# Optimization experiments

Measured on AMD Instinct MI355X. Metric: run time of the kernel, lower is better.

Reference implementation:

```python
import jax, jax.numpy as jnp
import numpy as np

B, D, H, O = 4096, 1024, 8192, 1000

def _l2norm_rows(w):
    return w / jnp.maximum(jnp.linalg.norm(w, axis=1, keepdims=True), 1e-12)

def setup_inputs() -> dict:
    key = jax.random.key(0)
    k1, k2, k3 = jax.random.split(key, 3)
    x = jax.random.normal(k1, (B, D), dtype=jnp.float32)
    kohonen_weights = _l2norm_rows(jax.random.normal(k2, (H, D), dtype=jnp.float32))
    grossberg_weights = _l2norm_rows(jax.random.normal(k3, (O, H), dtype=jnp.float32))
    return {"x": x, "kohonen_weights": kohonen_weights, "grossberg_weights": grossberg_weights}

def reference(x, kohonen_weights, grossberg_weights):
    # x: [B, D] (already flat), kohonen_weights: [H, D], grossberg_weights: [O, H]
    x2 = jnp.sum(x * x, axis=1, keepdims=True)              # [B, 1]
    w2 = jnp.sum(kohonen_weights * kohonen_weights, axis=1)  # [H]
    # Euclidean cdist via the expanded quadratic form (same as torch.cdist p=2)
    sq = x2 + w2[None, :] - 2.0 * (x @ kohonen_weights.T)    # [B, H]
    distances = jnp.sqrt(jnp.maximum(sq, 0.0))
    winners = jnp.argmin(distances, axis=1)                  # [B] int
    # one_hot @ grossberg_weights.T is exactly a row gather of grossberg_weights.T
    output = jnp.take(grossberg_weights.T, winners, axis=0)  # [B, O]
    return (output, winners)
```

## Files before the change

kernel.cpp:

```cpp
#include <hip/hip_runtime.h>
#include <hip/hip_bf16.h>
#include <hip/hip_fp16.h>


#define BB 4096
#define DD 1024
#define HH 8192
#define OO 1000

#define BM 256
#define BN 128
#define BK 64
#define NTILES (HH / BN)

typedef _Float16 f16;
typedef float f32x4 __attribute__((ext_vector_type(4)));

typedef __attribute__((address_space(3))) uint32_t lds_u32_t;
typedef __attribute__((address_space(1))) uint32_t glb_u32_t;

__device__ __forceinline__ uint32_t packkey(float v, int col) {
  uint32_t u = __float_as_uint(v);
  uint32_t mask = (uint32_t)((int32_t)u >> 31) | 0x80000000u;
  u ^= mask;
  return (u & 0xFFFFFF80u) | (uint32_t)col;
}
__device__ __forceinline__ float unpackval(uint32_t k) {
  uint32_t u = k & 0xFFFFFF80u;
  uint32_t mask = (k & 0x80000000u) ? 0x80000000u : 0xFFFFFFFFu;
  return __uint_as_float(u ^ mask);
}
__device__ __forceinline__ void kmerge(uint32_t& k1, uint32_t& k2,
                                       uint32_t o1, uint32_t o2) {
  uint32_t mn = min(k1, o1);
  uint32_t alt = (k1 > o1) ? k2 : o2;
  k1 = max(k1, o1);
  k2 = max(mn, alt);
}

__global__ __launch_bounds__(256) void cvt_kernel(
    const float* __restrict__ x, const float* __restrict__ kw,
    uint8_t* __restrict__ xq, uint8_t* __restrict__ kq,
    const float* __restrict__ G, float* __restrict__ Gt) {
  const int tid = threadIdx.x;
  const int blk = blockIdx.x;
  __shared__ float tile[32][33];
  if (blk < (BB + HH) / 4) {
#pragma unroll
    for (int i = 0; i < 4; ++i) {
      int r = blk * 4 + i;
      const float* src = (r < BB) ? (x + (size_t)r * DD)
                                  : (kw + (size_t)(r - BB) * DD);
      uint8_t* dst = (r < BB) ? (xq + (size_t)r * DD)
                              : (kq + (size_t)(r - BB) * DD);
      float4 v = ((const float4*)src)[tid];
      int p = 0;
      p = __builtin_amdgcn_cvt_pk_fp8_f32(v.x, v.y, p, false);
      p = __builtin_amdgcn_cvt_pk_fp8_f32(v.z, v.w, p, true);
      ((int*)dst)[tid] = p;
    }
  } else {
    if (Gt == nullptr) return;
    const int tb = blk - (BB + HH) / 4;
    const int tx = tid & 31;
    const int ty = tid >> 5;
#pragma unroll 1
    for (int j4 = 0; j4 < 4; ++j4) {
      int tile_id = tb * 4 + j4;
      int h0 = (tile_id >> 5) * 32;
      int o0 = (tile_id & 31) * 32;
      __syncthreads();
#pragma unroll
      for (int j = 0; j < 4; ++j) {
        int o = o0 + ty + j * 8;
        if (o < OO) tile[ty + j * 8][tx] = G[(size_t)o * HH + h0 + tx];
      }
      __syncthreads();
#pragma unroll
      for (int j = 0; j < 4; ++j) {
        int o = o0 + tx;
        int h = h0 + ty + j * 8;
        if (o < OO) Gt[(size_t)h * OO + o] = tile[tx][ty + j * 8];
      }
    }
  }
}

__global__ __launch_bounds__(256, 2) void gemm_top2(
    const uint8_t* __restrict__ A, const uint8_t* __restrict__ Bt,
    uint4* __restrict__ pk) {
  __shared__ __align__(16) uint8_t sA[BM * BK];
  __shared__ __align__(16) uint8_t sB[BN * BK];
  __shared__ uint2 mk[BM][2];

  const int tid = threadIdx.x;
  const int w = tid >> 6;
  const int L = tid & 63;

  const int bid = blockIdx.y * gridDim.x + blockIdx.x;
  const int c8 = bid & 7;
  const int tt = bid >> 3;
  const int nx = c8 * 8 + (tt & 7);
  const int my = tt >> 3;
  const int m0 = my * BM;
  const int n0 = nx * BN;

  const int wr = w >> 1;
  const int wc = w & 1;

  f32x4 acc[8][4];
#pragma unroll
  for (int i = 0; i < 8; ++i)
#pragma unroll
    for (int j = 0; j < 4; ++j) {
      acc[i][j][0] = 0.f; acc[i][j][1] = 0.f; acc[i][j][2] = 0.f; acc[i][j][3] = 0.f;
    }

  const int lm = L & 15;
  const int lq = L >> 4;

  const uint8_t* pA[4]; int dA[4];
#pragma unroll
  for (int j = 0; j < 4; ++j) {
    int c = tid + 256 * j;
    int r = c >> 2;
    int so = ((c & 3) ^ ((r >> 1) & 3)) * 16;
    pA[j] = A + (size_t)(m0 + r) * DD + so;
    dA[j] = c * 16;
  }
  const uint8_t* pB[2]; int dB[2];
#pragma unroll
  for (int j = 0; j < 2; ++j) {
    int c = tid + 256 * j;
    int r = c >> 2;
    int so = ((c & 3) ^ ((r >> 1) & 3)) * 16;
    pB[j] = Bt + (size_t)(n0 + r) * DD + so;
    dB[j] = c * 16;
  }

  const int t2 = (lm >> 1) & 3;
  const int raBase = (wr * 128 + lm) * BK;
  const int rbBase = (wc * 64 + lm) * BK;
  const int off0 = (((lq >> 1)) ^ t2) * 16 + (lq & 1) * 8;
  const int off1 = ((2 + (lq >> 1)) ^ t2) * 16 + (lq & 1) * 8;

  for (int kt = 0; kt < DD / BK; ++kt) {
    __syncthreads();
#pragma unroll
    for (int j = 0; j < 4; ++j) {
      __builtin_amdgcn_global_load_lds((const glb_u32_t*)pA[j], (lds_u32_t*)(sA + dA[j]), 16, 0, 0);
      pA[j] += BK;
    }
#pragma unroll
    for (int j = 0; j < 2; ++j) {
      __builtin_amdgcn_global_load_lds((const glb_u32_t*)pB[j], (lds_u32_t*)(sB + dB[j]), 16, 0, 0);
      pB[j] += BK;
    }
    __syncthreads();

    long long af[8], bf[4];
#pragma unroll
    for (int i = 0; i < 8; ++i)
      af[i] = *(const long long*)(sA + raBase + i * 16 * BK + off0);
#pragma unroll
    for (int j = 0; j < 4; ++j)
      bf[j] = *(const long long*)(sB + rbBase + j * 16 * BK + off0);
#pragma unroll
    for (int i = 0; i < 8; ++i)
#pragma unroll
      for (int j = 0; j < 4; ++j)
        acc[i][j] = __builtin_amdgcn_mfma_f32_16x16x32_fp8_fp8(af[i], bf[j], acc[i][j], 0, 0, 0);
#pragma unroll
    for (int i = 0; i < 8; ++i)
      af[i] = *(const long long*)(sA + raBase + i * 16 * BK + off1);
#pragma unroll
    for (int j = 0; j < 4; ++j)
      bf[j] = *(const long long*)(sB + rbBase + j * 16 * BK + off1);
#pragma unroll
    for (int i = 0; i < 8; ++i)
#pragma unroll
      for (int j = 0; j < 4; ++j)
        acc[i][j] = __builtin_amdgcn_mfma_f32_16x16x32_fp8_fp8(af[i], bf[j], acc[i][j], 0, 0, 0);
  }

  const int col0 = wc * 64 + lm;
#pragma unroll
  for (int i = 0; i < 8; ++i) {
#pragma unroll
    for (int r = 0; r < 4; ++r) {
      uint32_t k1 = 0, k2 = 0;
#pragma unroll
      for (int j = 0; j < 4; ++j) {
        uint32_t kj = packkey(acc[i][j][r], col0 + j * 16);
        if (kj > k1) { k2 = k1; k1 = kj; }
        else k2 = max(k2, kj);
      }
#pragma unroll
      for (int msk = 1; msk < 16; msk <<= 1) {
        uint32_t o1 = (uint32_t)__shfl_xor((int)k1, msk, 64);
        uint32_t o2 = (uint32_t)__shfl_xor((int)k2, msk, 64);
        kmerge(k1, k2, o1, o2);
      }
      if (lm == 0) {
        int rl = wr * 128 + i * 16 + lq * 4 + r;
        mk[rl][wc] = make_uint2(k1, k2);
      }
    }
  }
  __syncthreads();
  {
    uint2 a = mk[tid][0], b = mk[tid][1];
    pk[(size_t)(m0 + tid) * NTILES + nx] = make_uint4(a.x, a.y, b.x, b.y);
  }
}

__global__ __launch_bounds__(256) void select_kernel(
    const float* __restrict__ x, const float* __restrict__ kw,
    const uint4* __restrict__ pk,
    const float* __restrict__ Gt, const float* __restrict__ G,
    float* __restrict__ out, float* __restrict__ out_w) {
  const int b = blockIdx.x * 4 + (threadIdx.x >> 6);
  const int L = threadIdx.x & 63;

  const float4* x4 = (const float4*)(x + (size_t)b * DD);
  float4 xv[4];
#pragma unroll
  for (int j = 0; j < 4; ++j) xv[j] = x4[L + 64 * j];

  uint4 kp = pk[(size_t)b * NTILES + L];

  double x2 = 0.0;
#pragma unroll
  for (int j = 0; j < 4; ++j)
    x2 += (double)xv[j].x * xv[j].x + (double)xv[j].y * xv[j].y +
          (double)xv[j].z * xv[j].z + (double)xv[j].w * xv[j].w;
#pragma unroll
  for (int msk = 1; msk < 64; msk <<= 1) x2 += __shfl_xor(x2, msk, 64);

  uint32_t m = max(kp.x, kp.z);
#pragma unroll
  for (int msk = 1; msk < 64; msk <<= 1)
    m = max(m, (uint32_t)__shfl_xor((int)m, msk, 64));
  const uint32_t thrk = packkey(unpackval(m) - 0.35f, 0);

  unsigned long long cand[4];
  cand[0] = __ballot(kp.x >= thrk);
  cand[1] = __ballot(kp.y >= thrk);
  cand[2] = __ballot(kp.z >= thrk);
  cand[3] = __ballot(kp.w >= thrk);

  double best = 1e300;
  int bestc = 0x7fffffff;
#pragma unroll 1
  for (int pass = 0; pass < 4; ++pass) {
    unsigned long long bits = cand[pass];
    uint32_t mykey = (pass == 0) ? kp.x : (pass == 1) ? kp.y
                    : (pass == 2) ? kp.z : kp.w;
    while (bits) {
      int tt = __ffsll((long long)bits) - 1;
      bits &= bits - 1;
      uint32_t kbt = (uint32_t)__shfl((int)mykey, tt, 64);
      int col = tt * 128 + (int)(kbt & 127u);
      const float4* k4 = (const float4*)(kw + (size_t)col * DD);
      double dot = 0.0, w2 = 0.0;
#pragma unroll
      for (int j = 0; j < 4; ++j) {
        float4 wv = k4[L + 64 * j];
        dot += (double)xv[j].x * wv.x + (double)xv[j].y * wv.y +
               (double)xv[j].z * wv.z + (double)xv[j].w * wv.w;
        w2 += (double)wv.x * wv.x + (double)wv.y * wv.y +
              (double)wv.z * wv.z + (double)wv.w * wv.w;
      }
#pragma unroll
      for (int msk = 1; msk < 64; msk <<= 1) {
        dot += __shfl_xor(dot, msk, 64);
        w2 += __shfl_xor(w2, msk, 64);
      }
      double sq = x2 + w2 - 2.0 * dot;
      if (sq < best || (sq == best && col < bestc)) { best = sq; bestc = col; }
    }
  }

  if (L == 0) out_w[b] = (float)bestc;
  if (Gt != nullptr) {
    const float4* gsrc = (const float4*)(Gt + (size_t)bestc * OO);
    float4* gdst = (float4*)(out + (size_t)b * OO);
#pragma unroll
    for (int j = 0; j < 4; ++j) {
      int q = L + 64 * j;
      if (q < OO / 4) gdst[q] = gsrc[q];
    }
  } else {
#pragma unroll 1
    for (int j = 0; j < 16; ++j) {
      int o = L + 64 * j;
      if (o < OO) out[(size_t)b * OO + o] = G[(size_t)o * HH + bestc];
    }
  }
}

extern "C" void kernel_launch(void* const* d_in, const int* in_sizes, int n_in,
                              void* d_out, int out_size, void* d_ws, size_t ws_size,
                              hipStream_t stream) {
  const float* x  = (const float*)d_in[0];
  const float* kw = (const float*)d_in[1];
  const float* gw = (const float*)d_in[2];
  float* out = (float*)d_out;
  float* out_w = out + (size_t)BB * OO;

  const size_t MB = 1024 * 1024;
  char* ws = (char*)d_ws;
  uint8_t* xq = (uint8_t*)(ws);
  uint8_t* kq = (uint8_t*)(ws + 4 * MB);
  uint4*   pk = (uint4*)(ws + 12 * MB);
  float*   Gt = (float*)(ws + 16 * MB);
  const size_t need = 16 * MB + sizeof(float) * (size_t)HH * OO;
  float* GtArg = (ws_size >= need) ? Gt : nullptr;

  int cvt_blocks = (BB + HH) / 4 + (GtArg ? 2048 : 0);
  cvt_kernel<<<cvt_blocks, 256, 0, stream>>>(x, kw, xq, kq, gw, GtArg);

  dim3 g(HH / BN, BB / BM);
  gemm_top2<<<g, 256, 0, stream>>>(xq, kq, pk);

  select_kernel<<<BB / 4, 256, 0, stream>>>(x, kw, pk, GtArg, gw, out, out_w);
}
```

Baseline: 218.9 us.

## Triple-buffer LDS tiles with async global-to-LDS prefetch and finer swizzle

Turns the single-buffered GEMM main loop into a 3-stage LDS ring. Tiles are prefetched two iterations ahead with global_load_lds, and manual vmcnt waits replace the double __syncthreads, so global loads overlap MFMA work. The quantize kernel also gains an extra XOR swizzle of 8-byte halves keyed on row bit 3, with matching LDS read offsets, to reduce LDS bank conflicts. It adds s_setprio around the compute phase. LDS use rises to 3x for the tiles, which could limit the 2-blocks-per-CU occupancy.

```diff
diff --git a/kernel.cpp b/kernel.cpp
--- a/kernel.cpp
+++ b/kernel.cpp
@@ -12,6 +12,8 @@
 #define BN 128
 #define BK 64
 #define NTILES (HH / BN)
+#define SA_TILE (BM * BK)
+#define SB_TILE (BN * BK)
 
 typedef _Float16 f16;
 typedef float f32x4 __attribute__((ext_vector_type(4)));
@@ -57,7 +59,8 @@
       int p = 0;
       p = __builtin_amdgcn_cvt_pk_fp8_f32(v.x, v.y, p, false);
       p = __builtin_amdgcn_cvt_pk_fp8_f32(v.z, v.w, p, true);
-      ((int*)dst)[tid] = p;
+      int wi = tid ^ (((r >> 3) & 1) << 1);
+      ((int*)dst)[wi] = p;
     }
   } else {
     if (Gt == nullptr) return;
@@ -89,8 +92,8 @@
 __global__ __launch_bounds__(256, 2) void gemm_top2(
     const uint8_t* __restrict__ A, const uint8_t* __restrict__ Bt,
     uint4* __restrict__ pk) {
-  __shared__ __align__(16) uint8_t sA[BM * BK];
-  __shared__ __align__(16) uint8_t sB[BN * BK];
+  __shared__ __align__(16) uint8_t sA[3][SA_TILE];
+  __shared__ __align__(16) uint8_t sB[3][SB_TILE];
   __shared__ uint2 mk[BM][2];
 
   const int tid = threadIdx.x;
@@ -138,33 +141,53 @@
     dB[j] = c * 16;
   }
 
+  auto stage = [&](int t, int p) {
+#pragma unroll
+    for (int j = 0; j < 4; ++j)
+      __builtin_amdgcn_global_load_lds((const glb_u32_t*)(pA[j] + (size_t)t * BK),
+                                       (lds_u32_t*)(&sA[p][0] + dA[j]), 16, 0, 0);
+#pragma unroll
+    for (int j = 0; j < 2; ++j)
+      __builtin_amdgcn_global_load_lds((const glb_u32_t*)(pB[j] + (size_t)t * BK),
+                                       (lds_u32_t*)(&sB[p][0] + dB[j]), 16, 0, 0);
+  };
+
   const int t2 = (lm >> 1) & 3;
+  const int s3 = (lm >> 3) & 1;
   const int raBase = (wr * 128 + lm) * BK;
   const int rbBase = (wc * 64 + lm) * BK;
-  const int off0 = (((lq >> 1)) ^ t2) * 16 + (lq & 1) * 8;
-  const int off1 = ((2 + (lq >> 1)) ^ t2) * 16 + (lq & 1) * 8;
-
+  const int off0 = ((lq >> 1) ^ t2) * 16 + ((lq & 1) ^ s3) * 8;
+  const int off1 = ((2 + (lq >> 1)) ^ t2) * 16 + ((lq & 1) ^ s3) * 8;
+
+  stage(0, 0);
+  stage(1, 1);
+
+  int cur = 0;
+#pragma unroll 1
   for (int kt = 0; kt < DD / BK; ++kt) {
-    __syncthreads();
-#pragma unroll
-    for (int j = 0; j < 4; ++j) {
-      __builtin_amdgcn_global_load_lds((const glb_u32_t*)pA[j], (lds_u32_t*)(sA + dA[j]), 16, 0, 0);
-      pA[j] += BK;
-    }
-#pragma unroll
-    for (int j = 0; j < 2; ++j) {
-      __builtin_amdgcn_global_load_lds((const glb_u32_t*)pB[j], (lds_u32_t*)(sB + dB[j]), 16, 0, 0);
-      pB[j] += BK;
-    }
-    __syncthreads();
-
+    if (kt == DD / BK - 1)
+      asm volatile("s_waitcnt vmcnt(0) lgkmcnt(0)" ::: "memory");
+    else
+      asm volatile("s_waitcnt vmcnt(6) lgkmcnt(0)" ::: "memory");
+    __builtin_amdgcn_s_barrier();
+    asm volatile("" ::: "memory");
+
+    if (kt < DD / BK - 2) {
+      int stp = cur + 2; if (stp >= 3) stp -= 3;
+      stage(kt + 2, stp);
+    }
+
+    const uint8_t* bufA = &sA[cur][0];
+    const uint8_t* bufB = &sB[cur][0];
+
+    __builtin_amdgcn_s_setprio(1);
     long long af[8], bf[4];
 #pragma unroll
     for (int i = 0; i < 8; ++i)
-      af[i] = *(const long long*)(sA + raBase + i * 16 * BK + off0);
+      af[i] = *(const long long*)(bufA + raBase + i * 16 * BK + off0);
 #pragma unroll
     for (int j = 0; j < 4; ++j)
-      bf[j] = *(const long long*)(sB + rbBase + j * 16 * BK + off0);
+      bf[j] = *(const long long*)(bufB + rbBase + j * 16 * BK + off0);
 #pragma unroll
     for (int i = 0; i < 8; ++i)
 #pragma unroll
@@ -172,15 +195,18 @@
         acc[i][j] = __builtin_amdgcn_mfma_f32_16x16x32_fp8_fp8(af[i], bf[j], acc[i][j], 0, 0, 0);
 #pragma unroll
     for (int i = 0; i < 8; ++i)
-      af[i] = *(const long long*)(sA + raBase + i * 16 * BK + off1);
+      af[i] = *(const long long*)(bufA + raBase + i * 16 * BK + off1);
 #pragma unroll
     for (int j = 0; j < 4; ++j)
-      bf[j] = *(const long long*)(sB + rbBase + j * 16 * BK + off1);
+      bf[j] = *(const long long*)(bufB + rbBase + j * 16 * BK + off1);
 #pragma unroll
     for (int i = 0; i < 8; ++i)
 #pragma unroll
       for (int j = 0; j < 4; ++j)
         acc[i][j] = __builtin_amdgcn_mfma_f32_16x16x32_fp8_fp8(af[i], bf[j], acc[i][j], 0, 0, 0);
+    __builtin_amdgcn_s_setprio(0);
+
+    cur = (cur == 2) ? 0 : cur + 1;
   }
 
   const int col0 = wc * 64 + lm;
```

Measured after the change: 222.8 us. Within noise of the previous version (+1.8%).
